# Optimization experiments

Hardware: AMD Instinct MI355X
Metric: run time of the kernel (lower is better)

Reference implementation:

```python
import jax, jax.numpy as jnp
import numpy as np

D_MODEL = 1024
N_HEADS = 16
D_K = D_MODEL // N_HEADS
LN_EPS = 1e-5
NEG = -1e9


def setup_inputs() -> dict:
    key = jax.random.key(0)
    ks = jax.random.split(key, 12)
    B, S = 4, 2048
    s = 1.0 / np.sqrt(D_MODEL)
    # causal mask (1 = keep, 0 = masked)
    causal = jnp.tril(jnp.ones((S, S), dtype=jnp.int32))
    mask = jnp.broadcast_to(causal[None, None], (B, 1, S, S))
    return {
        "Q": jax.random.normal(ks[0], (B, S, D_MODEL), jnp.float32),
        "K": jax.random.normal(ks[1], (B, S, D_MODEL), jnp.float32),
        "V": jax.random.normal(ks[2], (B, S, D_MODEL), jnp.float32),
        "mask": mask,
        "Wq": jax.random.normal(ks[3], (D_MODEL, D_MODEL), jnp.float32) * s,
        "bq": jnp.zeros((D_MODEL,), jnp.float32),
        "Wk": jax.random.normal(ks[4], (D_MODEL, D_MODEL), jnp.float32) * s,
        "bk": jnp.zeros((D_MODEL,), jnp.float32),
        "Wv": jax.random.normal(ks[5], (D_MODEL, D_MODEL), jnp.float32) * s,
        "bv": jnp.zeros((D_MODEL,), jnp.float32),
        "Wo": jax.random.normal(ks[6], (D_MODEL, D_MODEL), jnp.float32) * s,
        "bo": jnp.zeros((D_MODEL,), jnp.float32),
        "ln_gamma": jnp.ones((D_MODEL,), jnp.float32),
        "ln_beta": jnp.zeros((D_MODEL,), jnp.float32),
    }


def _split_heads(x, B, S):
    # (B,S,D) -> (B,H,S,d_k)
    return x.reshape(B, S, N_HEADS, D_K).transpose(0, 2, 1, 3)


def reference(Q, K, V, mask, Wq, bq, Wk, bk, Wv, bv, Wo, bo, ln_gamma, ln_beta):
    B, S, _ = Q.shape
    residual = Q
    q = _split_heads(Q @ Wq + bq, B, S)
    k = _split_heads(K @ Wk + bk, B, S)
    v = _split_heads(V @ Wv + bv, B, S)
    scores = jnp.einsum("bhqd,bhkd->bhqk", q, k) / np.sqrt(D_K).astype(np.float32)
    scores = jnp.where(mask == 0, jnp.float32(NEG), scores)
    attn = jax.nn.softmax(scores, axis=-1)  # dropout p=0 -> identity
    ctx = jnp.einsum("bhqk,bhkd->bhqd", attn, v)
    ctx = ctx.transpose(0, 2, 1, 3).reshape(B, S, D_MODEL)
    out = ctx @ Wo + bo
    x = out + residual
    mu = jnp.mean(x, axis=-1, keepdims=True)
    var = jnp.mean(jnp.square(x - mu), axis=-1, keepdims=True)
    y = (x - mu) * jax.lax.rsqrt(var + LN_EPS) * ln_gamma + ln_beta
    return (y, attn)
```

## Files before the change

kernel.cpp:

```cpp
#include <hip/hip_runtime.h>

#define D_MODEL 1024
#define NH 16
#define DKH 64
#define SEQ 2048
#define BATCH 4
#define ROWS (BATCH*SEQ)

typedef _Float16 f16;
typedef _Float16 f16x4 __attribute__((ext_vector_type(4)));
typedef _Float16 f16x8 __attribute__((ext_vector_type(8)));
typedef float f32x4 __attribute__((ext_vector_type(4)));

#define MFMA16(a,b,c) __builtin_amdgcn_mfma_f32_16x16x32_f16((a),(b),(c),0,0,0)

__device__ __forceinline__ void gload16(const void* g, void* l) {
  __builtin_amdgcn_global_load_lds((const __attribute__((address_space(1))) void*)g,
                                   (__attribute__((address_space(3))) void*)l,
                                   16, 0, 0);
}


__global__ __launch_bounds__(256) void cvt_w_kernel(const float* __restrict__ Wq,
    const float* __restrict__ Wk, const float* __restrict__ Wv, const float* __restrict__ Wo,
    f16* __restrict__ dst)
{
  const float* W = (blockIdx.z==0)?Wq:(blockIdx.z==1)?Wk:(blockIdx.z==2)?Wv:Wo;
  f16* d = dst + (size_t)blockIdx.z * ((size_t)D_MODEL*D_MODEL);
  int idx = blockIdx.x*256 + threadIdx.x;
  int k = idx>>10, n = idx&1023;
  d[(size_t)n*D_MODEL + k] = (f16)W[idx];
}


template<int AF32>
__global__ __launch_bounds__(256) void gemm128(
    const void* __restrict__ A0, const void* __restrict__ A1, const void* __restrict__ A2,
    const f16* __restrict__ WTbase,
    const float* __restrict__ bias0, const float* __restrict__ bias1, const float* __restrict__ bias2,
    f16* __restrict__ out0, f16* __restrict__ out1, f16* __restrict__ out2,
    const float* __restrict__ resid, float* __restrict__ xout, int modeBase)
{
  __shared__ f16 Al[2][128*32];
  __shared__ f16 Bl[2][128*32];
  const int t = threadIdx.x, w = t>>6, l = t&63;
  const int nwg = (int)gridDim.x;
  const int wg = ((int)blockIdx.x & 7) * (nwg >> 3) + ((int)blockIdx.x >> 3);
  const int z  = wg >> 9;
  const int r2 = wg & 511;
  const int bm = r2 >> 3, bn = r2 & 7;
  const int mode = modeBase + z;
  const f16* WT = WTbase + (size_t)mode * ((size_t)D_MODEL*D_MODEL);
  const float* bias = (mode==0)?bias0:(mode==1)?bias1:(mode==2)?bias2:bias0;
  const int wm = w>>1, wn = w&1;
  const int lr = l>>2, lc = l&3, fr = l&15, fg = l>>4;
  f32x4 acc[4][4] = {};
  const char* Bb = (const char*)(WT + (size_t)bn*128*D_MODEL);

#define STAGEB(bufv, ktv) do { \
    char* Bd = (char*)&Bl[0][0] + (bufv)*8192; \
    _Pragma("unroll") \
    for (int cc=0; cc<2; ++cc) { \
      int r0 = w*32 + cc*16; \
      gload16(Bb + (size_t)(r0+lr)*2048 + (ktv)*64 + lc*16, Bd + r0*64); \
    } \
  } while(0)

#define COMPUTEK(bufv) do { \
    const f16* Ac = (const f16*)((char*)&Al[0][0] + (bufv)*8192); \
    const f16* Bc = (const f16*)((char*)&Bl[0][0] + (bufv)*8192); \
    f16x8 a[4], b[4]; \
    _Pragma("unroll") \
    for (int i=0;i<4;++i) a[i] = *(const f16x8*)(Ac + (wm*64+i*16+fr)*32 + fg*8); \
    _Pragma("unroll") \
    for (int j=0;j<4;++j) b[j] = *(const f16x8*)(Bc + (wn*64+j*16+fr)*32 + fg*8); \
    _Pragma("unroll") \
    for (int i=0;i<4;++i) \
      _Pragma("unroll") \
      for (int j=0;j<4;++j) \
        acc[i][j] = MFMA16(a[i], b[j], acc[i][j]); \
  } while(0)

  if constexpr (AF32) {
    const float* A32 = (const float*)((z==0)?A0:(z==1)?A1:A2);
    const float* Arow = A32 + (size_t)(bm*128 + w*32 + (l>>2))*1024 + (l&3)*8;
    f32x4 la[2][2];
    auto LOADA = [&](int ktv) {
      #pragma unroll
      for (int s=0;s<2;++s)
        #pragma unroll
        for (int q=0;q<2;++q)
          la[s][q] = *(const f32x4*)(Arow + (size_t)s*16*1024 + ktv*32 + q*4);
    };
    auto WRITEA = [&](int bufv) {
      char* Ad = (char*)&Al[0][0] + bufv*8192 + w*2048 + l*16;
      #pragma unroll
      for (int s=0;s<2;++s) {
        f16x8 pk;
        #pragma unroll
        for (int q=0;q<2;++q)
          #pragma unroll
          for (int m=0;m<4;++m) pk[q*4+m] = (f16)la[s][q][m];
        *(f16x8*)(Ad + s*1024) = pk;
      }
    };
    LOADA(0); STAGEB(0, 0); WRITEA(0);
    __syncthreads();
    for (int kt=0; kt<31; ++kt) {
      const int cur = kt & 1;
      LOADA(kt+1);
      STAGEB(cur^1, kt+1);
      COMPUTEK(cur);
      WRITEA(cur^1);
      __syncthreads();
    }
    COMPUTEK(1);
  } else {
    const char* Ab = (const char*)((const f16*)A0 + (size_t)bm*128*D_MODEL);
    auto STAGEA = [&](int bufv, int ktv) {
      char* Ad = (char*)&Al[0][0] + bufv*8192;
      #pragma unroll
      for (int cc=0; cc<2; ++cc) {
        int r0 = w*32 + cc*16;
        gload16(Ab + (size_t)(r0+lr)*2048 + ktv*64 + lc*16, Ad + r0*64);
      }
    };
    STAGEA(0,0); STAGEB(0, 0);
    asm volatile("s_waitcnt vmcnt(0)" ::: "memory");
    __builtin_amdgcn_s_barrier();
    for (int kt=0; kt<31; ++kt) {
      const int cur = kt & 1;
      STAGEA(cur^1, kt+1);
      STAGEB(cur^1, kt+1);
      COMPUTEK(cur);
      asm volatile("s_waitcnt vmcnt(0)" ::: "memory");
      __builtin_amdgcn_s_barrier();
    }
    COMPUTEK(1);
  }

#undef STAGEB
#undef COMPUTEK

  #pragma unroll
  for (int j=0;j<4;++j) {
    int col = bn*128 + wn*64 + j*16 + fr;
    float bz = bias[col];
    #pragma unroll
    for (int i=0;i<4;++i) {
      int row0 = bm*128 + wm*64 + i*16 + fg*4;
      f32x4 v = acc[i][j];
      if (mode==0) {
        int hh = col>>6, dk = col&63;
        #pragma unroll
        for (int r=0;r<4;++r) {
          int row = row0+r; int b_ = row>>11, s = row&(SEQ-1);
          out0[((size_t)(b_*NH+hh)*SEQ + s)*DKH + dk] = (f16)((v[r]+bz)*0.125f);
        }
      } else if (mode==1) {
        int hh = col>>6, dk = col&63;
        #pragma unroll
        for (int r=0;r<4;++r) {
          int row = row0+r; int b_ = row>>11, s = row&(SEQ-1);
          out1[((size_t)(b_*NH+hh)*SEQ + s)*DKH + dk] = (f16)(v[r]+bz);
        }
      } else if (mode==2) {
        int hh = col>>6, dk = col&63;
        int b_ = row0>>11, s0 = row0&(SEQ-1);
        f16x4 pk;
        #pragma unroll
        for (int r=0;r<4;++r) pk[r] = (f16)(v[r]+bz);
        *(f16x4*)(out2 + ((size_t)(b_*NH+hh)*DKH + dk)*SEQ + s0) = pk;
      } else {
        #pragma unroll
        for (int r=0;r<4;++r) {
          size_t o = (size_t)(row0+r)*D_MODEL + col;
          xout[o] = v[r] + bz + resid[o];
        }
      }
    }
  }
}


__global__ __launch_bounds__(256) void attn_kernel(
    const f16* __restrict__ qws, const f16* __restrict__ kws, const f16* __restrict__ vTws,
    float* __restrict__ attn, f16* __restrict__ ctx)
{
  __shared__ f16 el[4][32*128];
  const int t = threadIdx.x, w = t>>6, l = t&63;
  const int wg = ((int)blockIdx.x & 7)*64 + ((int)blockIdx.x >> 3);
  const int bh = wg >> 3;
  const int pr = wg & 7;
  const int qtA = pr, qtB = 15 - pr;
  const int fr = l & 15, fg = l >> 4;
  const f16* kp = kws + (size_t)bh*SEQ*DKH;
  const f16* vp = vTws + (size_t)bh*DKH*SEQ;
  const f16* qpA = qws + ((size_t)bh*SEQ + (size_t)qtA*128)*DKH;
  const f16* qpB = qws + ((size_t)bh*SEQ + (size_t)qtB*128)*DKH;
  float* apA = attn + ((size_t)bh*SEQ + (size_t)qtA*128)*SEQ;
  float* apB = attn + ((size_t)bh*SEQ + (size_t)qtB*128)*SEQ;
  f16* elw = (f16*)&el[w][0];
  const int swzx = (fr & 7) << 2;
  const int rbrow = l >> 5;
  const int rbslot = l & 31;

  f16x8 qfA[2][2], qfB[2][2];
  #pragma unroll
  for (int i=0;i<2;++i)
    #pragma unroll
    for (int kc=0;kc<2;++kc) {
      qfA[i][kc] = *(const f16x8*)(qpA + (w*32 + i*16 + fr)*DKH + kc*32 + fg*8);
      qfB[i][kc] = *(const f16x8*)(qpB + (w*32 + i*16 + fr)*DKH + kc*32 + fg*8);
    }

  auto fill_tile = [&](float* apr, int kt2) {
    f32x4 z4 = {0.f,0.f,0.f,0.f};
    #pragma unroll
    for (int i2=0;i2<16;++i2) {
      int idx = t + i2*256;
      int row = idx >> 5, c4 = idx & 31;
      __builtin_nontemporal_store(z4, (f32x4*)(apr + (size_t)row*SEQ + (size_t)kt2*128 + c4*4));
    }
  };
  const int cB = pr;

  auto pass1_tile = [&](int ktv, bool diag, const f16x8 (&qf)[2][2], float (&psum)[2]) {
    const f16* kb = kp + (size_t)ktv*128*DKH;
    #pragma unroll
    for (int jh=0; jh<2; ++jh) {
      f32x4 sc[2][4] = {};
      #pragma unroll
      for (int j2=0;j2<4;++j2) {
        const int j = jh*4 + j2;
        #pragma unroll
        for (int kc=0;kc<2;++kc) {
          f16x8 kf = *(const f16x8*)(kb + (j*16+fr)*DKH + kc*32 + fg*8);
          sc[0][j2] = MFMA16(kf, qf[0][kc], sc[0][j2]);
          sc[1][j2] = MFMA16(kf, qf[1][kc], sc[1][j2]);
        }
      }
      if (diag) {
        #pragma unroll
        for (int i=0;i<2;++i) {
          int rloc = w*32 + i*16 + fr;
          #pragma unroll
          for (int j2=0;j2<4;++j2)
            #pragma unroll
            for (int r=0;r<4;++r) {
              int cloc = (jh*4+j2)*16 + fg*4 + r;
              if (cloc <= rloc) psum[i] += __expf(sc[i][j2][r]);
            }
        }
      } else {
        #pragma unroll
        for (int i=0;i<2;++i)
          #pragma unroll
          for (int j2=0;j2<4;++j2)
            #pragma unroll
            for (int r=0;r<4;++r) psum[i] += __expf(sc[i][j2][r]);
      }
    }
  };

  float psumA[2] = {0.f,0.f}, psumB[2] = {0.f,0.f};
  int u = 0, f = 0;
  auto drip_fills = [&]() {
    while (f*17 < u*15) {
      if (f < cB) fill_tile(apB, qtB+1+f);
      else        fill_tile(apA, qtA+1+(f-cB));
      ++f;
    }
  };
  for (int kt=0; kt<=qtB; ++kt) { pass1_tile(kt, kt==qtB, qfB, psumB); ++u; drip_fills(); }
  for (int kt=0; kt<=qtA; ++kt) { pass1_tile(kt, kt==qtA, qfA, psumA); ++u; drip_fills(); }

  #pragma unroll
  for (int m=16; m<64; m<<=1) {
    psumA[0] += __shfl_xor(psumA[0], m, 64);
    psumA[1] += __shfl_xor(psumA[1], m, 64);
    psumB[0] += __shfl_xor(psumB[0], m, 64);
    psumB[1] += __shfl_xor(psumB[1], m, 64);
  }
  float rinvA[2] = {1.f/psumA[0], 1.f/psumA[1]};
  float rinvB[2] = {1.f/psumB[0], 1.f/psumB[1]};

  f32x4 av[2][4];
  auto pass2_tile = [&](int ktv, bool diag, const f16x8 (&qf)[2][2], const float (&rinv)[2], float* apr) {
    const f16* kb = kp + (size_t)ktv*128*DKH;
    #pragma unroll
    for (int jh=0; jh<2; ++jh) {
      f32x4 sc[2][4] = {};
      #pragma unroll
      for (int j2=0;j2<4;++j2) {
        const int j = jh*4 + j2;
        #pragma unroll
        for (int kc=0;kc<2;++kc) {
          f16x8 kf = *(const f16x8*)(kb + (j*16+fr)*DKH + kc*32 + fg*8);
          sc[0][j2] = MFMA16(kf, qf[0][kc], sc[0][j2]);
          sc[1][j2] = MFMA16(kf, qf[1][kc], sc[1][j2]);
        }
      }
      #pragma unroll
      for (int i=0;i<2;++i) {
        const int rloc = w*32 + i*16 + fr;
        #pragma unroll
        for (int j2=0;j2<4;++j2) {
          const int j = jh*4 + j2;
          f16x4 ef;
          #pragma unroll
          for (int r=0;r<4;++r) {
            int cloc = j*16 + fg*4 + r;
            float e = (diag && cloc > rloc) ? 0.f : __expf(sc[i][j2][r]) * rinv[i];
            ef[r] = (f16)e;
          }
          *(f16x4*)(elw + (i*16+fr)*128 + (((j*4+fg) ^ swzx) << 2)) = ef;
        }
      }
    }
    {
      float* apk = apr + (size_t)(w*32)*SEQ + (size_t)ktv*128;
      #pragma unroll
      for (int p=0;p<16;++p) {
        int row = p*2 + rbrow;
        f16x4 pv4 = *(const f16x4*)(elw + row*128 + ((rbslot ^ ((row&7)<<2)) << 2));
        f32x4 o4; o4[0]=(float)pv4[0]; o4[1]=(float)pv4[1]; o4[2]=(float)pv4[2]; o4[3]=(float)pv4[3];
        __builtin_nontemporal_store(o4, (f32x4*)(apk + (size_t)row*SEQ + rbslot*4));
      }
    }
    #pragma unroll
    for (int c=0;c<4;++c) {
      f16x8 pf0 = *(const f16x8*)(elw + (fr)*128    + (((c*8+fg*2) ^ swzx) << 2));
      f16x8 pf1 = *(const f16x8*)(elw + (16+fr)*128 + (((c*8+fg*2) ^ swzx) << 2));
      #pragma unroll
      for (int j2=0;j2<4;++j2) {
        f16x8 vf = *(const f16x8*)(vp + (j2*16+fr)*SEQ + ktv*128 + c*32 + fg*8);
        av[0][j2] = MFMA16(vf, pf0, av[0][j2]);
        av[1][j2] = MFMA16(vf, pf1, av[1][j2]);
      }
    }
  };
  auto ctx_store = [&](int qtv) {
    const int b_ = bh >> 4, hh = bh & 15;
    #pragma unroll
    for (int i=0;i<2;++i) {
      size_t rowoff = ((size_t)b_*SEQ + (size_t)qtv*128 + w*32 + i*16 + fr) * D_MODEL + hh*DKH;
      #pragma unroll
      for (int j2=0;j2<4;++j2) {
        f16x4 pk;
        #pragma unroll
        for (int r=0;r<4;++r) pk[r] = (f16)av[i][j2][r];
        *(f16x4*)(ctx + rowoff + j2*16 + fg*4) = pk;
      }
    }
  };

  #pragma unroll
  for (int i=0;i<2;++i)
    #pragma unroll
    for (int j2=0;j2<4;++j2) av[i][j2] = (f32x4){0.f,0.f,0.f,0.f};
  for (int kt=0; kt<=qtA; ++kt) pass2_tile(kt, kt==qtA, qfA, rinvA, apA);
  ctx_store(qtA);

  #pragma unroll
  for (int i=0;i<2;++i)
    #pragma unroll
    for (int j2=0;j2<4;++j2) av[i][j2] = (f32x4){0.f,0.f,0.f,0.f};
  for (int kt=0; kt<=qtB; ++kt) pass2_tile(kt, kt==qtB, qfB, rinvB, apB);
  ctx_store(qtB);
}


__global__ __launch_bounds__(256) void ln_kernel(const float* __restrict__ x,
    const float* __restrict__ gamma, const float* __restrict__ beta, float* __restrict__ y)
{
  __shared__ float red[4];
  __shared__ float red2[4];
  const int t = threadIdx.x, w = t>>6, l = t&63;
  const size_t row = blockIdx.x;
  float4 v = ((const float4*)(x + row*D_MODEL))[t];
  float s = v.x+v.y+v.z+v.w;
  #pragma unroll
  for (int m=1;m<64;m<<=1) s += __shfl_xor(s, m, 64);
  if (l==0) red[w] = s;
  __syncthreads();
  float mu = (red[0]+red[1]+red[2]+red[3]) * (1.f/D_MODEL);
  float dx=v.x-mu, dy=v.y-mu, dz=v.z-mu, dw=v.w-mu;
  float q = dx*dx+dy*dy+dz*dz+dw*dw;
  #pragma unroll
  for (int m=1;m<64;m<<=1) q += __shfl_xor(q, m, 64);
  if (l==0) red2[w] = q;
  __syncthreads();
  float var = (red2[0]+red2[1]+red2[2]+red2[3]) * (1.f/D_MODEL);
  float rs = rsqrtf(var + 1e-5f);
  float4 g  = ((const float4*)gamma)[t];
  float4 bb = ((const float4*)beta)[t];
  float4 o;
  o.x = dx*rs*g.x + bb.x;
  o.y = dy*rs*g.y + bb.y;
  o.z = dz*rs*g.z + bb.z;
  o.w = dw*rs*g.w + bb.w;
  ((float4*)(y + row*D_MODEL))[t] = o;
}


extern "C" void kernel_launch(void* const* d_in, const int* in_sizes, int n_in,
                              void* d_out, int out_size, void* d_ws, size_t ws_size,
                              hipStream_t stream)
{
  const float* Q  = (const float*)d_in[0];
  const float* K  = (const float*)d_in[1];
  const float* V  = (const float*)d_in[2];
  const float* Wq = (const float*)d_in[4];
  const float* bq = (const float*)d_in[5];
  const float* Wk = (const float*)d_in[6];
  const float* bk = (const float*)d_in[7];
  const float* Wv = (const float*)d_in[8];
  const float* bv = (const float*)d_in[9];
  const float* Wo = (const float*)d_in[10];
  const float* bo = (const float*)d_in[11];
  const float* gam= (const float*)d_in[12];
  const float* bet= (const float*)d_in[13];

  float* y    = (float*)d_out;
  float* attn = y + (size_t)ROWS*D_MODEL;

  char* ws = (char*)d_ws;
  const size_t SZ = (size_t)ROWS*D_MODEL*sizeof(f16);
  f16* ctx   = (f16*)ws;
  float* xb  = (float*)(ws + SZ);
  f16* WT    = (f16*)(ws + 3*SZ);
  f16* qws   = (f16*)(ws + 3*SZ + ((size_t)4*D_MODEL*D_MODEL*sizeof(f16)));
  f16* kws   = (f16*)((char*)qws + SZ);
  f16* vT    = (f16*)((char*)kws + SZ);

  cvt_w_kernel<<<dim3(4096,1,4), 256, 0, stream>>>(Wq, Wk, Wv, Wo, WT);
  gemm128<1><<<1536, 256, 0, stream>>>(Q, K, V, WT, bq, bk, bv, qws, kws, vT, nullptr, nullptr, 0);
  attn_kernel<<<512, 256, 0, stream>>>(qws, kws, vT, attn, ctx);
  gemm128<0><<<512, 256, 0, stream>>>(ctx, nullptr, nullptr, WT, bo, bo, bo, nullptr, nullptr, nullptr, Q, xb, 3);
  ln_kernel<<<8192, 256, 0, stream>>>(xb, gam, bet, y);
}
```

Measured before the change: 484.4 us.

## Split attention block into 8 waves of 16 query rows each

Doubles the attention kernel's block from 256 to 512 threads so each wave handles 16 query rows instead of 32, halving per-wave register state for Q fragments, scores and accumulators. The aim is more waves in flight to hide the latency of global K/V fragment loads and the large attn stores. In exchange, each K and V fragment is now loaded by twice as many waves, raising L1/L2 traffic, and the MFMA work per load drops.

```diff
diff --git a/kernel.cpp b/kernel.cpp
--- a/kernel.cpp
+++ b/kernel.cpp
@@ -183,17 +183,18 @@
 }
 
 
-__global__ __launch_bounds__(256) void attn_kernel(
+__global__ __launch_bounds__(512, 4) void attn_kernel(
     const f16* __restrict__ qws, const f16* __restrict__ kws, const f16* __restrict__ vTws,
     float* __restrict__ attn, f16* __restrict__ ctx)
 {
-  __shared__ f16 el[4][32*128];
+  __shared__ f16 el[8][16*128];
   const int t = threadIdx.x, w = t>>6, l = t&63;
   const int wg = ((int)blockIdx.x & 7)*64 + ((int)blockIdx.x >> 3);
   const int bh = wg >> 3;
   const int pr = wg & 7;
   const int qtA = pr, qtB = 15 - pr;
   const int fr = l & 15, fg = l >> 4;
+  const int lrow = w*16 + fr;
   const f16* kp = kws + (size_t)bh*SEQ*DKH;
   const f16* vp = vTws + (size_t)bh*DKH*SEQ;
   const f16* qpA = qws + ((size_t)bh*SEQ + (size_t)qtA*128)*DKH;
@@ -205,65 +206,56 @@
   const int rbrow = l >> 5;
   const int rbslot = l & 31;
 
-  f16x8 qfA[2][2], qfB[2][2];
-  #pragma unroll
-  for (int i=0;i<2;++i)
-    #pragma unroll
-    for (int kc=0;kc<2;++kc) {
-      qfA[i][kc] = *(const f16x8*)(qpA + (w*32 + i*16 + fr)*DKH + kc*32 + fg*8);
-      qfB[i][kc] = *(const f16x8*)(qpB + (w*32 + i*16 + fr)*DKH + kc*32 + fg*8);
-    }
+  f16x8 qfA[2], qfB[2];
+  #pragma unroll
+  for (int kc=0;kc<2;++kc) {
+    qfA[kc] = *(const f16x8*)(qpA + lrow*DKH + kc*32 + fg*8);
+    qfB[kc] = *(const f16x8*)(qpB + lrow*DKH + kc*32 + fg*8);
+  }
 
   auto fill_tile = [&](float* apr, int kt2) {
     f32x4 z4 = {0.f,0.f,0.f,0.f};
     #pragma unroll
-    for (int i2=0;i2<16;++i2) {
-      int idx = t + i2*256;
+    for (int i2=0;i2<8;++i2) {
+      int idx = t + i2*512;
       int row = idx >> 5, c4 = idx & 31;
       __builtin_nontemporal_store(z4, (f32x4*)(apr + (size_t)row*SEQ + (size_t)kt2*128 + c4*4));
     }
   };
   const int cB = pr;
 
-  auto pass1_tile = [&](int ktv, bool diag, const f16x8 (&qf)[2][2], float (&psum)[2]) {
+  auto pass1_slice = [&](int ktv, bool diag, const f16x8 (&qf)[2], float& psum) {
     const f16* kb = kp + (size_t)ktv*128*DKH;
     #pragma unroll
     for (int jh=0; jh<2; ++jh) {
-      f32x4 sc[2][4] = {};
+      f32x4 sc[4] = {};
       #pragma unroll
       for (int j2=0;j2<4;++j2) {
         const int j = jh*4 + j2;
         #pragma unroll
         for (int kc=0;kc<2;++kc) {
           f16x8 kf = *(const f16x8*)(kb + (j*16+fr)*DKH + kc*32 + fg*8);
-          sc[0][j2] = MFMA16(kf, qf[0][kc], sc[0][j2]);
-          sc[1][j2] = MFMA16(kf, qf[1][kc], sc[1][j2]);
+          sc[j2] = MFMA16(kf, qf[kc], sc[j2]);
         }
       }
       if (diag) {
         #pragma unroll
-        for (int i=0;i<2;++i) {
-          int rloc = w*32 + i*16 + fr;
+        for (int j2=0;j2<4;++j2)
           #pragma unroll
-          for (int j2=0;j2<4;++j2)
-            #pragma unroll
-            for (int r=0;r<4;++r) {
-              int cloc = (jh*4+j2)*16 + fg*4 + r;
-              if (cloc <= rloc) psum[i] += __expf(sc[i][j2][r]);
-            }
-        }
+          for (int r=0;r<4;++r) {
+            int cloc = (jh*4+j2)*16 + fg*4 + r;
+            if (cloc <= lrow) psum += __expf(sc[j2][r]);
+          }
       } else {
         #pragma unroll
-        for (int i=0;i<2;++i)
+        for (int j2=0;j2<4;++j2)
           #pragma unroll
-          for (int j2=0;j2<4;++j2)
-            #pragma unroll
-            for (int r=0;r<4;++r) psum[i] += __expf(sc[i][j2][r]);
+          for (int r=0;r<4;++r) psum += __expf(sc[j2][r]);
       }
     }
   };
 
-  float psumA[2] = {0.f,0.f}, psumB[2] = {0.f,0.f};
+  float psumA = 0.f, psumB = 0.f;
   int u = 0, f = 0;
   auto drip_fills = [&]() {
     while (f*17 < u*15) {
@@ -272,56 +264,48 @@
       ++f;
     }
   };
-  for (int kt=0; kt<=qtB; ++kt) { pass1_tile(kt, kt==qtB, qfB, psumB); ++u; drip_fills(); }
-  for (int kt=0; kt<=qtA; ++kt) { pass1_tile(kt, kt==qtA, qfA, psumA); ++u; drip_fills(); }
+  for (int kt=0; kt<=qtB; ++kt) { pass1_slice(kt, kt==qtB, qfB, psumB); ++u; drip_fills(); }
+  for (int kt=0; kt<=qtA; ++kt) { pass1_slice(kt, kt==qtA, qfA, psumA); ++u; drip_fills(); }
 
   #pragma unroll
   for (int m=16; m<64; m<<=1) {
-    psumA[0] += __shfl_xor(psumA[0], m, 64);
-    psumA[1] += __shfl_xor(psumA[1], m, 64);
-    psumB[0] += __shfl_xor(psumB[0], m, 64);
-    psumB[1] += __shfl_xor(psumB[1], m, 64);
+    psumA += __shfl_xor(psumA, m, 64);
+    psumB += __shfl_xor(psumB, m, 64);
   }
-  float rinvA[2] = {1.f/psumA[0], 1.f/psumA[1]};
-  float rinvB[2] = {1.f/psumB[0], 1.f/psumB[1]};
-
-  f32x4 av[2][4];
-  auto pass2_tile = [&](int ktv, bool diag, const f16x8 (&qf)[2][2], const float (&rinv)[2], float* apr) {
+  float rinvA = 1.f/psumA, rinvB = 1.f/psumB;
+
+  f32x4 av[4];
+  auto pass2_slice = [&](int ktv, bool diag, const f16x8 (&qf)[2], float rinv, float* apr) {
     const f16* kb = kp + (size_t)ktv*128*DKH;
     #pragma unroll
     for (int jh=0; jh<2; ++jh) {
-      f32x4 sc[2][4] = {};
+      f32x4 sc[4] = {};
       #pragma unroll
       for (int j2=0;j2<4;++j2) {
         const int j = jh*4 + j2;
         #pragma unroll
         for (int kc=0;kc<2;++kc) {
           f16x8 kf = *(const f16x8*)(kb + (j*16+fr)*DKH + kc*32 + fg*8);
-          sc[0][j2] = MFMA16(kf, qf[0][kc], sc[0][j2]);
-          sc[1][j2] = MFMA16(kf, qf[1][kc], sc[1][j2]);
-        }
-      }
-      #pragma unroll
-      for (int i=0;i<2;++i) {
-        const int rloc = w*32 + i*16 + fr;
-        #pragma unroll
-        for (int j2=0;j2<4;++j2) {
-          const int j = jh*4 + j2;
-          f16x4 ef;
-          #pragma unroll
-          for (int r=0;r<4;++r) {
-            int cloc = j*16 + fg*4 + r;
-            float e = (diag && cloc > rloc) ? 0.f : __expf(sc[i][j2][r]) * rinv[i];
-            ef[r] = (f16)e;
-          }
-          *(f16x4*)(elw + (i*16+fr)*128 + (((j*4+fg) ^ swzx) << 2)) = ef;
-        }
+          sc[j2] = MFMA16(kf, qf[kc], sc[j2]);
+        }
+      }
+      #pragma unroll
+      for (int j2=0;j2<4;++j2) {
+        const int j = jh*4 + j2;
+        f16x4 ef;
+        #pragma unroll
+        for (int r=0;r<4;++r) {
+          int cloc = j*16 + fg*4 + r;
+          float e = (diag && cloc > lrow) ? 0.f : __expf(sc[j2][r]) * rinv;
+          ef[r] = (f16)e;
+        }
+        *(f16x4*)(elw + fr*128 + (((j*4+fg) ^ swzx) << 2)) = ef;
       }
     }
     {
-      float* apk = apr + (size_t)(w*32)*SEQ + (size_t)ktv*128;
-      #pragma unroll
-      for (int p=0;p<16;++p) {
+      float* apk = apr + (size_t)(w*16)*SEQ + (size_t)ktv*128;
+      #pragma unroll
+      for (int p=0;p<8;++p) {
         int row = p*2 + rbrow;
         f16x4 pv4 = *(const f16x4*)(elw + row*128 + ((rbslot ^ ((row&7)<<2)) << 2));
         f32x4 o4; o4[0]=(float)pv4[0]; o4[1]=(float)pv4[1]; o4[2]=(float)pv4[2]; o4[3]=(float)pv4[3];
@@ -330,43 +314,34 @@
     }
     #pragma unroll
     for (int c=0;c<4;++c) {
-      f16x8 pf0 = *(const f16x8*)(elw + (fr)*128    + (((c*8+fg*2) ^ swzx) << 2));
-      f16x8 pf1 = *(const f16x8*)(elw + (16+fr)*128 + (((c*8+fg*2) ^ swzx) << 2));
+      f16x8 pf = *(const f16x8*)(elw + fr*128 + (((c*8+fg*2) ^ swzx) << 2));
       #pragma unroll
       for (int j2=0;j2<4;++j2) {
         f16x8 vf = *(const f16x8*)(vp + (j2*16+fr)*SEQ + ktv*128 + c*32 + fg*8);
-        av[0][j2] = MFMA16(vf, pf0, av[0][j2]);
-        av[1][j2] = MFMA16(vf, pf1, av[1][j2]);
+        av[j2] = MFMA16(vf, pf, av[j2]);
       }
     }
   };
   auto ctx_store = [&](int qtv) {
     const int b_ = bh >> 4, hh = bh & 15;
-    #pragma unroll
-    for (int i=0;i<2;++i) {
-      size_t rowoff = ((size_t)b_*SEQ + (size_t)qtv*128 + w*32 + i*16 + fr) * D_MODEL + hh*DKH;
-      #pragma unroll
-      for (int j2=0;j2<4;++j2) {
-        f16x4 pk;
-        #pragma unroll
-        for (int r=0;r<4;++r) pk[r] = (f16)av[i][j2][r];
-        *(f16x4*)(ctx + rowoff + j2*16 + fg*4) = pk;
-      }
+    size_t rowoff = ((size_t)b_*SEQ + (size_t)qtv*128 + lrow) * D_MODEL + hh*DKH;
+    #pragma unroll
+    for (int j2=0;j2<4;++j2) {
+      f16x4 pk;
+      #pragma unroll
+      for (int r=0;r<4;++r) pk[r] = (f16)av[j2][r];
+      *(f16x4*)(ctx + rowoff + j2*16 + fg*4) = pk;
     }
   };
 
   #pragma unroll
-  for (int i=0;i<2;++i)
-    #pragma unroll
-    for (int j2=0;j2<4;++j2) av[i][j2] = (f32x4){0.f,0.f,0.f,0.f};
-  for (int kt=0; kt<=qtA; ++kt) pass2_tile(kt, kt==qtA, qfA, rinvA, apA);
+  for (int j2=0;j2<4;++j2) av[j2] = (f32x4){0.f,0.f,0.f,0.f};
+  for (int kt=0; kt<=qtA; ++kt) pass2_slice(kt, kt==qtA, qfA, rinvA, apA);
   ctx_store(qtA);
 
   #pragma unroll
-  for (int i=0;i<2;++i)
-    #pragma unroll
-    for (int j2=0;j2<4;++j2) av[i][j2] = (f32x4){0.f,0.f,0.f,0.f};
-  for (int kt=0; kt<=qtB; ++kt) pass2_tile(kt, kt==qtB, qfB, rinvB, apB);
+  for (int j2=0;j2<4;++j2) av[j2] = (f32x4){0.f,0.f,0.f,0.f};
+  for (int kt=0; kt<=qtB; ++kt) pass2_slice(kt, kt==qtB, qfB, rinvB, apB);
   ctx_store(qtB);
 }
 
@@ -436,7 +411,7 @@
 
   cvt_w_kernel<<<dim3(4096,1,4), 256, 0, stream>>>(Wq, Wk, Wv, Wo, WT);
   gemm128<1><<<1536, 256, 0, stream>>>(Q, K, V, WT, bq, bk, bv, qws, kws, vT, nullptr, nullptr, 0);
-  attn_kernel<<<512, 256, 0, stream>>>(qws, kws, vT, attn, ctx);
+  attn_kernel<<<512, 512, 0, stream>>>(qws, kws, vT, attn, ctx);
   gemm128<0><<<512, 256, 0, stream>>>(ctx, nullptr, nullptr, WT, bo, bo, bo, nullptr, nullptr, nullptr, Q, xb, 3);
   ln_kernel<<<8192, 256, 0, stream>>>(xb, gam, bet, y);
 }
```

Result: slower. 559.2 us (+15.4%).

## Share K-tile loads across paired query tiles in pass 1 and raise MFMA priority

Applied to the files above, without the earlier changes.

Pass 1 (row-sum of exponentials) now walks the shared key tiles 0..qtA once, computing scores for both paired query tiles A and B from the same K fragment, then finishes B's remaining tiles separately. This halves K fragment loads for the overlapping range and gives more independent MFMAs per load. The drip-fill pacing ratio now uses B's tile count instead of a constant. s_setprio is also wrapped around the MFMA blocks in pass 2 so waves issuing matrix work get scheduling priority; the combined loop raises register pressure.

```diff
diff --git a/kernel.cpp b/kernel.cpp
--- a/kernel.cpp
+++ b/kernel.cpp
@@ -225,22 +225,43 @@
   };
   const int cB = pr;
 
-  auto pass1_tile = [&](int ktv, bool diag, const f16x8 (&qf)[2][2], float (&psum)[2]) {
-    const f16* kb = kp + (size_t)ktv*128*DKH;
+  float psumA[2] = {0.f,0.f}, psumB[2] = {0.f,0.f};
+  int u = 0, f = 0;
+  const int np1 = qtB + 1;
+  auto drip_fills = [&]() {
+    while (f*np1 < u*15) {
+      if (f < cB) fill_tile(apB, qtB+1+f);
+      else        fill_tile(apA, qtA+1+(f-cB));
+      ++f;
+    }
+  };
+
+  for (int kt=0; kt<=qtA; ++kt) {
+    const f16* kb = kp + (size_t)kt*128*DKH;
+    const bool diagA = (kt == qtA);
     #pragma unroll
     for (int jh=0; jh<2; ++jh) {
-      f32x4 sc[2][4] = {};
+      f32x4 scB[2][4] = {};
+      f32x4 scA[2][4] = {};
       #pragma unroll
       for (int j2=0;j2<4;++j2) {
         const int j = jh*4 + j2;
         #pragma unroll
         for (int kc=0;kc<2;++kc) {
           f16x8 kf = *(const f16x8*)(kb + (j*16+fr)*DKH + kc*32 + fg*8);
-          sc[0][j2] = MFMA16(kf, qf[0][kc], sc[0][j2]);
-          sc[1][j2] = MFMA16(kf, qf[1][kc], sc[1][j2]);
-        }
-      }
-      if (diag) {
+          scB[0][j2] = MFMA16(kf, qfB[0][kc], scB[0][j2]);
+          scB[1][j2] = MFMA16(kf, qfB[1][kc], scB[1][j2]);
+          scA[0][j2] = MFMA16(kf, qfA[0][kc], scA[0][j2]);
+          scA[1][j2] = MFMA16(kf, qfA[1][kc], scA[1][j2]);
+        }
+      }
+      #pragma unroll
+      for (int i=0;i<2;++i)
+        #pragma unroll
+        for (int j2=0;j2<4;++j2)
+          #pragma unroll
+          for (int r=0;r<4;++r) psumB[i] += __expf(scB[i][j2][r]);
+      if (diagA) {
         #pragma unroll
         for (int i=0;i<2;++i) {
           int rloc = w*32 + i*16 + fr;
@@ -249,7 +270,7 @@
             #pragma unroll
             for (int r=0;r<4;++r) {
               int cloc = (jh*4+j2)*16 + fg*4 + r;
-              if (cloc <= rloc) psum[i] += __expf(sc[i][j2][r]);
+              if (cloc <= rloc) psumA[i] += __expf(scA[i][j2][r]);
             }
         }
       } else {
@@ -258,22 +279,51 @@
           #pragma unroll
           for (int j2=0;j2<4;++j2)
             #pragma unroll
-            for (int r=0;r<4;++r) psum[i] += __expf(sc[i][j2][r]);
-      }
-    }
-  };
-
-  float psumA[2] = {0.f,0.f}, psumB[2] = {0.f,0.f};
-  int u = 0, f = 0;
-  auto drip_fills = [&]() {
-    while (f*17 < u*15) {
-      if (f < cB) fill_tile(apB, qtB+1+f);
-      else        fill_tile(apA, qtA+1+(f-cB));
-      ++f;
-    }
-  };
-  for (int kt=0; kt<=qtB; ++kt) { pass1_tile(kt, kt==qtB, qfB, psumB); ++u; drip_fills(); }
-  for (int kt=0; kt<=qtA; ++kt) { pass1_tile(kt, kt==qtA, qfA, psumA); ++u; drip_fills(); }
+            for (int r=0;r<4;++r) psumA[i] += __expf(scA[i][j2][r]);
+      }
+    }
+    ++u; drip_fills();
+  }
+
+  for (int kt=qtA+1; kt<=qtB; ++kt) {
+    const f16* kb = kp + (size_t)kt*128*DKH;
+    const bool diagB = (kt == qtB);
+    #pragma unroll
+    for (int jh=0; jh<2; ++jh) {
+      f32x4 sc[2][4] = {};
+      #pragma unroll
+      for (int j2=0;j2<4;++j2) {
+        const int j = jh*4 + j2;
+        #pragma unroll
+        for (int kc=0;kc<2;++kc) {
+          f16x8 kf = *(const f16x8*)(kb + (j*16+fr)*DKH + kc*32 + fg*8);
+          sc[0][j2] = MFMA16(kf, qfB[0][kc], sc[0][j2]);
+          sc[1][j2] = MFMA16(kf, qfB[1][kc], sc[1][j2]);
+        }
+      }
+      if (diagB) {
+        #pragma unroll
+        for (int i=0;i<2;++i) {
+          int rloc = w*32 + i*16 + fr;
+          #pragma unroll
+          for (int j2=0;j2<4;++j2)
+            #pragma unroll
+            for (int r=0;r<4;++r) {
+              int cloc = (jh*4+j2)*16 + fg*4 + r;
+              if (cloc <= rloc) psumB[i] += __expf(sc[i][j2][r]);
+            }
+        }
+      } else {
+        #pragma unroll
+        for (int i=0;i<2;++i)
+          #pragma unroll
+          for (int j2=0;j2<4;++j2)
+            #pragma unroll
+            for (int r=0;r<4;++r) psumB[i] += __expf(sc[i][j2][r]);
+      }
+    }
+    ++u; drip_fills();
+  }
 
   #pragma unroll
   for (int m=16; m<64; m<<=1) {
@@ -291,6 +341,7 @@
     #pragma unroll
     for (int jh=0; jh<2; ++jh) {
       f32x4 sc[2][4] = {};
+      __builtin_amdgcn_s_setprio(1);
       #pragma unroll
       for (int j2=0;j2<4;++j2) {
         const int j = jh*4 + j2;
@@ -301,6 +352,7 @@
           sc[1][j2] = MFMA16(kf, qf[1][kc], sc[1][j2]);
         }
       }
+      __builtin_amdgcn_s_setprio(0);
       #pragma unroll
       for (int i=0;i<2;++i) {
         const int rloc = w*32 + i*16 + fr;
@@ -328,6 +380,7 @@
         __builtin_nontemporal_store(o4, (f32x4*)(apk + (size_t)row*SEQ + rbslot*4));
       }
     }
+    __builtin_amdgcn_s_setprio(1);
     #pragma unroll
     for (int c=0;c<4;++c) {
       f16x8 pf0 = *(const f16x8*)(elw + (fr)*128    + (((c*8+fg*2) ^ swzx) << 2));
@@ -339,6 +392,7 @@
         av[1][j2] = MFMA16(vf, pf1, av[1][j2]);
       }
     }
+    __builtin_amdgcn_s_setprio(0);
   };
   auto ctx_store = [&](int qtv) {
     const int b_ = bh >> 4, hh = bh & 15;
```

Result: no change. 476.3 us (-1.7%).
